# Optimization experiments

Hardware: AMD Instinct MI355X
Metric: run time of the kernel (lower is better)

## Reference

```python
import jax, jax.numpy as jnp
import numpy as np

N_USER = 50000
N_ITEM = 50000
D_IN = 128
D_OUT = 128
N_EDGE = 600000


def _sage(x_src, x_dst, ei, Wl, bl, Wr):
    # PyG SAGEConv: out = lin_l(mean_{j in N(i)} x_j) + lin_r(x_i)
    # lin_l has bias, lin_r has no bias. Weights are [out, in].
    src, dst = ei[0], ei[1]
    n_dst = x_dst.shape[0]
    msg = x_src[src]                                            # [E, D_in] gather
    agg = jax.ops.segment_sum(msg, dst, num_segments=n_dst)     # [N_dst, D_in]
    cnt = jax.ops.segment_sum(jnp.ones((ei.shape[1],), x_src.dtype), dst,
                              num_segments=n_dst)
    mean = agg / jnp.maximum(cnt, 1.0)[:, None]                 # isolated nodes -> 0
    return mean @ Wl.T + bl + x_dst @ Wr.T


def setup_inputs() -> dict:
    key = jax.random.key(0)
    ks = jax.random.split(key, 16)
    inp = {
        "x_user": jax.random.normal(ks[0], (N_USER, D_IN), jnp.float32),
        "x_item": jax.random.normal(ks[1], (N_ITEM, D_IN), jnp.float32),
        "ei_rates": jax.random.randint(ks[2], (2, N_EDGE), 0, N_USER, jnp.int64 if jax.config.jax_enable_x64 else jnp.int32),
        "ei_rev": jax.random.randint(ks[3], (2, N_EDGE), 0, N_USER, jnp.int64 if jax.config.jax_enable_x64 else jnp.int32),
        "ei_follows": jax.random.randint(ks[4], (2, N_EDGE), 0, N_USER, jnp.int64 if jax.config.jax_enable_x64 else jnp.int32),
    }
    s = 1.0 / np.sqrt(D_IN)
    names = ["rates", "rev", "fol"]
    for i, nm in enumerate(names):
        inp[f"Wl_{nm}"] = jax.random.uniform(ks[5 + 3 * i], (D_OUT, D_IN), jnp.float32, -s, s)
        inp[f"bl_{nm}"] = jax.random.uniform(ks[6 + 3 * i], (D_OUT,), jnp.float32, -s, s)
        inp[f"Wr_{nm}"] = jax.random.uniform(ks[7 + 3 * i], (D_OUT, D_IN), jnp.float32, -s, s)
    return inp


def reference(x_user, x_item, ei_rates, ei_rev, ei_follows,
              Wl_rates, bl_rates, Wr_rates,
              Wl_rev, bl_rev, Wr_rev,
              Wl_fol, bl_fol, Wr_fol):
    # relation (user -rates-> item): src=user, dst=item
    out_item = _sage(x_user, x_item, ei_rates, Wl_rates, bl_rates, Wr_rates)
    # relation (item -rev_rates-> user): src=item, dst=user
    out_user_rev = _sage(x_item, x_user, ei_rev, Wl_rev, bl_rev, Wr_rev)
    # relation (user -follows-> user)
    out_user_fol = _sage(x_user, x_user, ei_follows, Wl_fol, bl_fol, Wr_fol)
    # HeteroConv aggr='mean': average relation outputs per dst node type
    out_user = (out_user_rev + out_user_fol) * 0.5
    return out_user, out_item
```

## Files before the change

kernel.cpp:

```cpp
#include <hip/hip_runtime.h>

#define D 128
#define NBB 392

typedef __attribute__((ext_vector_type(8))) short bf16x8;
typedef __attribute__((ext_vector_type(4))) float f32x4;

__device__ inline unsigned short f2bf(float f) {
  unsigned u = __builtin_bit_cast(unsigned, f);
  unsigned r = u + 0x7FFFu + ((u >> 16) & 1u);
  return (unsigned short)(r >> 16);
}
__device__ inline float bf2f(unsigned short b) {
  unsigned u = ((unsigned)b) << 16;
  return __builtin_bit_cast(float, u);
}

__global__ void __launch_bounds__(256) conv2_kernel(
    const float* __restrict__ xu, const float* __restrict__ xi,
    unsigned short* __restrict__ xbu, unsigned short* __restrict__ xbi,
    int n4u, int n4i) {
  int i = blockIdx.x * 256 + threadIdx.x;
  const float* x;
  unsigned short* xb;
  if (i < n4u) { x = xu; xb = xbu; }
  else { i -= n4u; if (i >= n4i) return; x = xi; xb = xbi; }
  float4 v = ((const float4*)x)[i];
  ushort4 o;
  o.x = f2bf(v.x); o.y = f2bf(v.y); o.z = f2bf(v.z); o.w = f2bf(v.w);
  ((ushort4*)xb)[i] = o;
}

struct Rel3 { const int* ei[3]; int ne[3]; int nb[3]; };

__global__ void __launch_bounds__(256) bhist_kernel(Rel3 R, int* __restrict__ bh) {
  int b = blockIdx.x, rel = 0;
  while (b >= R.nb[rel]) { b -= R.nb[rel]; rel++; }
  __shared__ int lh[NBB];
  for (int t = threadIdx.x; t < NBB; t += 256) lh[t] = 0;
  __syncthreads();
  const int ne = R.ne[rel];
  const int* dsts = R.ei[rel] + ne;
  const int base = b * 2048;
#pragma unroll
  for (int k = 0; k < 8; k++) {
    int i = base + k * 256 + threadIdx.x;
    if (i < ne) atomicAdd(&lh[dsts[i] >> 7], 1);
  }
  __syncthreads();
  for (int t = threadIdx.x; t < NBB; t += 256)
    if (lh[t]) atomicAdd(&bh[rel * NBB + t], lh[t]);
}

__global__ void __launch_bounds__(192) scanb_kernel(const int* __restrict__ bh,
                                                    int* __restrict__ bbase,
                                                    int* __restrict__ bcur, int nbkt) {
  int w = threadIdx.x >> 6, l = threadIdx.x & 63;
  if (w >= 3) return;
  const int off = w * NBB;
  int v[7];
  int s0 = 0;
#pragma unroll
  for (int k = 0; k < 7; k++) {
    int idx = l * 7 + k;
    v[k] = (idx < nbkt) ? bh[off + idx] : 0;
    s0 += v[k];
  }
  int s = s0;
  for (int dlt = 1; dlt < 64; dlt <<= 1) {
    int t = __shfl_up(s, dlt);
    if (l >= dlt) s += t;
  }
  int run = s - s0;
#pragma unroll
  for (int k = 0; k < 7; k++) {
    int idx = l * 7 + k;
    if (idx < nbkt) { bbase[off + idx] = run; bcur[off + idx] = run; run += v[k]; }
  }
  if (l == 63) bbase[off + nbkt] = run;
}

struct PArgs { const int* ei[3]; int ne[3]; int nb[3]; unsigned* part[3]; };

__global__ void __launch_bounds__(256) part_kernel(PArgs P, int* __restrict__ bcur,
                                                   int nbkt) {
  int b = blockIdx.x, rel = 0;
  while (b >= P.nb[rel]) { b -= P.nb[rel]; rel++; }
  const int ne = P.ne[rel];
  const int* src = P.ei[rel];
  const int* dst = src + ne;
  const int base = b * 4096;
  const int tn = min(4096, ne - base);
  __shared__ int lh[NBB], lscan[NBB], gb[NBB], lcur[NBB];
  __shared__ uint2 pairs[4096];
  const int tid = threadIdx.x;
  for (int t = tid; t < NBB; t += 256) lh[t] = 0;
  __syncthreads();
#pragma unroll
  for (int k = 0; k < 16; k++) {
    int i = base + k * 256 + tid;
    if (i < ne) atomicAdd(&lh[dst[i] >> 7], 1);
  }
  __syncthreads();
  if (tid < 64) {
    int v[7];
    int s0 = 0;
#pragma unroll
    for (int k = 0; k < 7; k++) {
      int idx = tid * 7 + k;
      v[k] = (idx < NBB) ? lh[idx] : 0;
      s0 += v[k];
    }
    int s = s0;
    for (int dlt = 1; dlt < 64; dlt <<= 1) {
      int t = __shfl_up(s, dlt);
      if (tid >= dlt) s += t;
    }
    int run = s - s0;
#pragma unroll
    for (int k = 0; k < 7; k++) {
      int idx = tid * 7 + k;
      if (idx < NBB) { lscan[idx] = run; run += v[k]; }
    }
  }
  __syncthreads();
  for (int t = tid; t < nbkt; t += 256) {
    gb[t] = atomicAdd(&bcur[rel * NBB + t], lh[t]);
    lcur[t] = lscan[t];
  }
  __syncthreads();
#pragma unroll
  for (int k = 0; k < 16; k++) {
    int i = base + k * 256 + tid;
    if (i < ne) {
      int d = dst[i];
      int slot = atomicAdd(&lcur[d >> 7], 1);
      pairs[slot] = (uint2){(unsigned)src[i], (unsigned)d};
    }
  }
  __syncthreads();
  unsigned* __restrict__ out = P.part[rel];
#pragma unroll
  for (int k = 0; k < 16; k++) {
    int slot = k * 256 + tid;
    if (slot < tn) {
      uint2 p = pairs[slot];
      int bin = (int)(p.y >> 7);
      out[gb[bin] + (slot - lscan[bin])] = p.x | ((p.y & 127u) << 25);
    }
  }
}

struct BAArgs {
  const unsigned* part[3];
  const unsigned short* xb[3];
  unsigned short* mean[3];
  int m[3];
};

__global__ void __launch_bounds__(256) bagg_kernel(BAArgs A, const int* __restrict__ bbase,
                                                   int nbkt) {
  const int rel = blockIdx.x / nbkt;
  const int b = blockIdx.x - rel * nbkt;
  const int bs = bbase[rel * NBB + b];
  const int be = bbase[rel * NBB + b + 1];
  const int n = be - bs;
  const unsigned* __restrict__ pp = A.part[rel] + bs;
  const unsigned short* __restrict__ x = A.xb[rel];
  unsigned short* __restrict__ mean = A.mean[rel];
  const int m = A.m[rel];
  const int tid = threadIdx.x;
  const int w = tid >> 6, lane = tid & 63;
  const size_t loff = lane * 2;
  __shared__ unsigned sorted[4096];
  __shared__ int lcnt[128], lofs[128], lcur[128];

  if (n <= 4096) {
    if (tid < 128) lcnt[tid] = 0;
    __syncthreads();
    for (int i = tid; i < n; i += 256) atomicAdd(&lcnt[pp[i] >> 25], 1);
    __syncthreads();
    if (tid < 64) {
      int v0 = lcnt[2 * tid], v1 = lcnt[2 * tid + 1];
      int s0 = v0 + v1, s = s0;
      for (int dlt = 1; dlt < 64; dlt <<= 1) {
        int t = __shfl_up(s, dlt);
        if (tid >= dlt) s += t;
      }
      int ex = s - s0;
      lofs[2 * tid] = ex;
      lofs[2 * tid + 1] = ex + v0;
    }
    __syncthreads();
    if (tid < 128) lcur[tid] = lofs[tid];
    __syncthreads();
    for (int i = tid; i < n; i += 256) {
      unsigned p = pp[i];
      int slot = atomicAdd(&lcur[p >> 25], 1);
      sorted[slot] = p & 0x1FFFFFFu;
    }
    __syncthreads();
    for (int r = w; r < 128; r += 4) {
      int gdst = b * 128 + r;
      if (gdst >= m) break;
      const int beg = lofs[r], end = lcur[r];
      float a0 = 0.f, a1 = 0.f, b0 = 0.f, b1 = 0.f;
      float c0 = 0.f, c1 = 0.f, d0 = 0.f, d1 = 0.f;
      int j = beg;
      for (; j + 4 <= end; j += 4) {
        unsigned s0 = sorted[j], s1 = sorted[j + 1], s2 = sorted[j + 2], s3 = sorted[j + 3];
        unsigned v0 = *(const unsigned*)(x + (size_t)s0 * D + loff);
        unsigned v1 = *(const unsigned*)(x + (size_t)s1 * D + loff);
        unsigned v2 = *(const unsigned*)(x + (size_t)s2 * D + loff);
        unsigned v3 = *(const unsigned*)(x + (size_t)s3 * D + loff);
        a0 += bf2f((unsigned short)(v0 & 0xFFFFu)); a1 += bf2f((unsigned short)(v0 >> 16));
        b0 += bf2f((unsigned short)(v1 & 0xFFFFu)); b1 += bf2f((unsigned short)(v1 >> 16));
        c0 += bf2f((unsigned short)(v2 & 0xFFFFu)); c1 += bf2f((unsigned short)(v2 >> 16));
        d0 += bf2f((unsigned short)(v3 & 0xFFFFu)); d1 += bf2f((unsigned short)(v3 >> 16));
      }
      for (; j < end; j++) {
        unsigned s = sorted[j];
        unsigned v = *(const unsigned*)(x + (size_t)s * D + loff);
        a0 += bf2f((unsigned short)(v & 0xFFFFu)); a1 += bf2f((unsigned short)(v >> 16));
      }
      a0 += (b0 + c0) + d0;
      a1 += (b1 + c1) + d1;
      float inv = 1.0f / (float)max(end - beg, 1);
      unsigned o = (unsigned)f2bf(a0 * inv) | ((unsigned)f2bf(a1 * inv) << 16);
      *(unsigned*)(mean + (size_t)gdst * D + loff) = o;
    }
  } else {
    for (int r = w; r < 128; r += 4) {
      int gdst = b * 128 + r;
      if (gdst >= m) break;
      float a0 = 0.f, a1 = 0.f;
      int cnt = 0;
      for (int j = 0; j < n; j++) {
        unsigned p = pp[j];
        if ((int)(p >> 25) == r) {
          unsigned v = *(const unsigned*)(x + (size_t)(p & 0x1FFFFFFu) * D + loff);
          a0 += bf2f((unsigned short)(v & 0xFFFFu));
          a1 += bf2f((unsigned short)(v >> 16));
          cnt++;
        }
      }
      float inv = 1.0f / (float)max(cnt, 1);
      unsigned o = (unsigned)f2bf(a0 * inv) | ((unsigned)f2bf(a1 * inv) << 16);
      *(unsigned*)(mean + (size_t)gdst * D + loff) = o;
    }
  }
}

__global__ void __launch_bounds__(384) prep_kernel(
    const float* __restrict__ Wl_rates, const float* __restrict__ Wr_rates, const float* __restrict__ bl_rates,
    const float* __restrict__ Wl_rev, const float* __restrict__ Wr_rev, const float* __restrict__ bl_rev,
    const float* __restrict__ Wl_fol, const float* __restrict__ Wr_fol, const float* __restrict__ bl_fol,
    unsigned short* __restrict__ Wb_user, unsigned short* __restrict__ Wb_item,
    float* __restrict__ b_user, float* __restrict__ b_item) {
  int n = blockIdx.x;
  int k = threadIdx.x;
  float v;
  if (k < 128)      v = 0.5f * Wl_rev[n * 128 + k];
  else if (k < 256) v = 0.5f * Wl_fol[n * 128 + (k - 128)];
  else              v = 0.5f * (Wr_rev[n * 128 + (k - 256)] + Wr_fol[n * 128 + (k - 256)]);
  Wb_user[n * 384 + k] = f2bf(v);
  if (k < 256) {
    float w = (k < 128) ? Wl_rates[n * 128 + k] : Wr_rates[n * 128 + (k - 128)];
    Wb_item[n * 256 + k] = f2bf(w);
  }
  if (n == 0 && k < 128) {
    b_item[k] = bl_rates[k];
    b_user[k] = 0.5f * (bl_rev[k] + bl_fol[k]);
  }
}

struct BSrcs { const unsigned short* s[3]; };
struct GemmArgs {
  BSrcs su, si;
  const unsigned short* wbU; const unsigned short* wbI;
  const float* bU; const float* bI;
  float* outU; float* outI;
  int MU, MI, nbU;
};

__global__ void __launch_bounds__(256) gemm2_kernel(GemmArgs A) {
  const bool isU = (int)blockIdx.x < A.nbU;
  const int bid = isU ? blockIdx.x : blockIdx.x - A.nbU;
  const BSrcs S = isU ? A.su : A.si;
  const unsigned short* __restrict__ Wb = isU ? A.wbU : A.wbI;
  const int K = isU ? 384 : 256;
  const float* __restrict__ bias = isU ? A.bU : A.bI;
  float* __restrict__ out = isU ? A.outU : A.outI;
  const int M = isU ? A.MU : A.MI;

  __shared__ __align__(16) unsigned short As[128][72];
  __shared__ __align__(16) unsigned short Ws[128][72];
  const int tid = threadIdx.x;
  const int lane = tid & 63;
  const int wave = tid >> 6;
  const int wr = (wave >> 1) * 64;
  const int wc = (wave & 1) * 64;
  const int l15 = lane & 15;
  const int quad = lane >> 4;
  const int m0 = bid * 128;

  f32x4 acc[4][4];
#pragma unroll
  for (int r = 0; r < 4; r++)
#pragma unroll
    for (int c = 0; c < 4; c++) acc[r][c] = (f32x4){0.f, 0.f, 0.f, 0.f};

  const int srow = tid >> 1, shalf = tid & 1;
  const int nchunks = K >> 6;
  for (int ch = 0; ch < nchunks; ch++) {
    const unsigned short* sp = S.s[ch >> 1];
    const int coff = (ch & 1) << 6;
    {
      int mm = min(m0 + srow, M - 1);
      const uint4* g = (const uint4*)(sp + (size_t)mm * D + coff + shalf * 32);
      uint4* ld = (uint4*)(&As[srow][shalf * 32]);
      ld[0] = g[0]; ld[1] = g[1]; ld[2] = g[2]; ld[3] = g[3];
    }
    {
      const uint4* g = (const uint4*)(Wb + (size_t)srow * K + ch * 64 + shalf * 32);
      uint4* ld = (uint4*)(&Ws[srow][shalf * 32]);
      ld[0] = g[0]; ld[1] = g[1]; ld[2] = g[2]; ld[3] = g[3];
    }
    __syncthreads();
#pragma unroll
    for (int kk = 0; kk < 64; kk += 32) {
      const int kb = kk + quad * 8;
      bf16x8 a0 = *(const bf16x8*)&As[wr + l15][kb];
      bf16x8 a1 = *(const bf16x8*)&As[wr + 16 + l15][kb];
      bf16x8 a2 = *(const bf16x8*)&As[wr + 32 + l15][kb];
      bf16x8 a3 = *(const bf16x8*)&As[wr + 48 + l15][kb];
      bf16x8 b0 = *(const bf16x8*)&Ws[wc + l15][kb];
      bf16x8 b1 = *(const bf16x8*)&Ws[wc + 16 + l15][kb];
      bf16x8 b2 = *(const bf16x8*)&Ws[wc + 32 + l15][kb];
      bf16x8 b3 = *(const bf16x8*)&Ws[wc + 48 + l15][kb];
      acc[0][0] = __builtin_amdgcn_mfma_f32_16x16x32_bf16(a0, b0, acc[0][0], 0, 0, 0);
      acc[0][1] = __builtin_amdgcn_mfma_f32_16x16x32_bf16(a0, b1, acc[0][1], 0, 0, 0);
      acc[0][2] = __builtin_amdgcn_mfma_f32_16x16x32_bf16(a0, b2, acc[0][2], 0, 0, 0);
      acc[0][3] = __builtin_amdgcn_mfma_f32_16x16x32_bf16(a0, b3, acc[0][3], 0, 0, 0);
      acc[1][0] = __builtin_amdgcn_mfma_f32_16x16x32_bf16(a1, b0, acc[1][0], 0, 0, 0);
      acc[1][1] = __builtin_amdgcn_mfma_f32_16x16x32_bf16(a1, b1, acc[1][1], 0, 0, 0);
      acc[1][2] = __builtin_amdgcn_mfma_f32_16x16x32_bf16(a1, b2, acc[1][2], 0, 0, 0);
      acc[1][3] = __builtin_amdgcn_mfma_f32_16x16x32_bf16(a1, b3, acc[1][3], 0, 0, 0);
      acc[2][0] = __builtin_amdgcn_mfma_f32_16x16x32_bf16(a2, b0, acc[2][0], 0, 0, 0);
      acc[2][1] = __builtin_amdgcn_mfma_f32_16x16x32_bf16(a2, b1, acc[2][1], 0, 0, 0);
      acc[2][2] = __builtin_amdgcn_mfma_f32_16x16x32_bf16(a2, b2, acc[2][2], 0, 0, 0);
      acc[2][3] = __builtin_amdgcn_mfma_f32_16x16x32_bf16(a2, b3, acc[2][3], 0, 0, 0);
      acc[3][0] = __builtin_amdgcn_mfma_f32_16x16x32_bf16(a3, b0, acc[3][0], 0, 0, 0);
      acc[3][1] = __builtin_amdgcn_mfma_f32_16x16x32_bf16(a3, b1, acc[3][1], 0, 0, 0);
      acc[3][2] = __builtin_amdgcn_mfma_f32_16x16x32_bf16(a3, b2, acc[3][2], 0, 0, 0);
      acc[3][3] = __builtin_amdgcn_mfma_f32_16x16x32_bf16(a3, b3, acc[3][3], 0, 0, 0);
    }
    __syncthreads();
  }
#pragma unroll
  for (int c = 0; c < 4; c++) {
    const int n = wc + c * 16 + l15;
    const float bv = bias[n];
#pragma unroll
    for (int r = 0; r < 4; r++) {
      const int mrow = m0 + wr + r * 16 + quad * 4;
#pragma unroll
      for (int i = 0; i < 4; i++) {
        if (mrow + i < M) out[(size_t)(mrow + i) * D + n] = acc[r][c][i] + bv;
      }
    }
  }
}

extern "C" void kernel_launch(void* const* d_in, const int* in_sizes, int n_in,
                              void* d_out, int out_size, void* d_ws, size_t ws_size,
                              hipStream_t stream) {
  const float* x_user   = (const float*)d_in[0];
  const float* x_item   = (const float*)d_in[1];
  const int*   ei_rates = (const int*)d_in[2];
  const int*   ei_rev   = (const int*)d_in[3];
  const int*   ei_fol   = (const int*)d_in[4];
  const float* Wl_rates = (const float*)d_in[5];
  const float* bl_rates = (const float*)d_in[6];
  const float* Wr_rates = (const float*)d_in[7];
  const float* Wl_rev   = (const float*)d_in[8];
  const float* bl_rev   = (const float*)d_in[9];
  const float* Wr_rev   = (const float*)d_in[10];
  const float* Wl_fol   = (const float*)d_in[11];
  const float* bl_fol   = (const float*)d_in[12];
  const float* Wr_fol   = (const float*)d_in[13];

  const int NU = in_sizes[0] / D;
  const int NI = in_sizes[1] / D;
  const int E_rates = in_sizes[2] / 2;
  const int E_rev   = in_sizes[3] / 2;
  const int E_fol   = in_sizes[4] / 2;
  const int nbkt = ((NU > NI ? NU : NI) + 127) / 128;

  char* wsb = (char*)d_ws;
  size_t off = 0;
  auto take = [&](size_t bytes) {
    char* p = wsb + off;
    off += (bytes + 15) & ~(size_t)15;
    return p;
  };
  int* bhist = (int*)take(3 * NBB * 4);
  const size_t zero_bytes = off;
  int* bbase = (int*)take(3 * NBB * 4);
  int* bcur  = (int*)take(3 * NBB * 4);
  unsigned* part_rates = (unsigned*)take((size_t)E_rates * 4);
  unsigned* part_rev   = (unsigned*)take((size_t)E_rev * 4);
  unsigned* part_fol   = (unsigned*)take((size_t)E_fol * 4);
  unsigned short* xb_user    = (unsigned short*)take((size_t)NU * D * 2);
  unsigned short* xb_item    = (unsigned short*)take((size_t)NI * D * 2);
  unsigned short* mean_rates = (unsigned short*)take((size_t)NI * D * 2);
  unsigned short* mean_rev   = (unsigned short*)take((size_t)NU * D * 2);
  unsigned short* mean_fol   = (unsigned short*)take((size_t)NU * D * 2);
  unsigned short* Wb_user    = (unsigned short*)take(128 * 384 * 2);
  unsigned short* Wb_item    = (unsigned short*)take(128 * 256 * 2);
  float* b_user = (float*)take(128 * 4);
  float* b_item = (float*)take(128 * 4);

  hipMemsetAsync(d_ws, 0, zero_bytes, stream);
  prep_kernel<<<128, 384, 0, stream>>>(Wl_rates, Wr_rates, bl_rates,
                                       Wl_rev, Wr_rev, bl_rev,
                                       Wl_fol, Wr_fol, bl_fol,
                                       Wb_user, Wb_item, b_user, b_item);
  {
    int n4u = NU * D / 4, n4i = NI * D / 4;
    conv2_kernel<<<(n4u + n4i + 255) / 256, 256, 0, stream>>>(
        x_user, x_item, xb_user, xb_item, n4u, n4i);
  }

  Rel3 R;
  R.ei[0] = ei_rates; R.ne[0] = E_rates; R.nb[0] = (E_rates + 2047) / 2048;
  R.ei[1] = ei_rev;   R.ne[1] = E_rev;   R.nb[1] = (E_rev + 2047) / 2048;
  R.ei[2] = ei_fol;   R.ne[2] = E_fol;   R.nb[2] = (E_fol + 2047) / 2048;
  bhist_kernel<<<R.nb[0] + R.nb[1] + R.nb[2], 256, 0, stream>>>(R, bhist);

  scanb_kernel<<<1, 192, 0, stream>>>(bhist, bbase, bcur, nbkt);

  PArgs P;
  P.ei[0] = ei_rates; P.ne[0] = E_rates; P.nb[0] = (E_rates + 4095) / 4096; P.part[0] = part_rates;
  P.ei[1] = ei_rev;   P.ne[1] = E_rev;   P.nb[1] = (E_rev + 4095) / 4096;   P.part[1] = part_rev;
  P.ei[2] = ei_fol;   P.ne[2] = E_fol;   P.nb[2] = (E_fol + 4095) / 4096;   P.part[2] = part_fol;
  part_kernel<<<P.nb[0] + P.nb[1] + P.nb[2], 256, 0, stream>>>(P, bcur, nbkt);

  BAArgs BA;
  BA.part[0] = part_rates; BA.xb[0] = xb_user; BA.mean[0] = mean_rates; BA.m[0] = NI;
  BA.part[1] = part_rev;   BA.xb[1] = xb_item; BA.mean[1] = mean_rev;   BA.m[1] = NU;
  BA.part[2] = part_fol;   BA.xb[2] = xb_user; BA.mean[2] = mean_fol;   BA.m[2] = NU;
  bagg_kernel<<<3 * nbkt, 256, 0, stream>>>(BA, bbase, nbkt);

  GemmArgs gma;
  gma.su.s[0] = mean_rev;   gma.su.s[1] = mean_fol; gma.su.s[2] = xb_user;
  gma.si.s[0] = mean_rates; gma.si.s[1] = xb_item;  gma.si.s[2] = nullptr;
  gma.wbU = Wb_user; gma.wbI = Wb_item;
  gma.bU = b_user;   gma.bI = b_item;
  gma.outU = (float*)d_out;
  gma.outI = (float*)d_out + (size_t)NU * D;
  gma.MU = NU; gma.MI = NI;
  gma.nbU = (NU + 127) / 128;
  const int nbI = (NI + 127) / 128;
  gemm2_kernel<<<gma.nbU + nbI, 256, 0, stream>>>(gma);
}
```

Before: 314.0 us.

## Merge setup kernels into one launch and interleave two rows in bucket aggregation

```diff
diff --git a/kernel.cpp b/kernel.cpp
--- a/kernel.cpp
+++ b/kernel.cpp
@@ -16,40 +16,71 @@
   return __builtin_bit_cast(float, u);
 }
 
-__global__ void __launch_bounds__(256) conv2_kernel(
-    const float* __restrict__ xu, const float* __restrict__ xi,
-    unsigned short* __restrict__ xbu, unsigned short* __restrict__ xbi,
-    int n4u, int n4i) {
-  int i = blockIdx.x * 256 + threadIdx.x;
-  const float* x;
-  unsigned short* xb;
-  if (i < n4u) { x = xu; xb = xbu; }
-  else { i -= n4u; if (i >= n4i) return; x = xi; xb = xbi; }
-  float4 v = ((const float4*)x)[i];
-  ushort4 o;
-  o.x = f2bf(v.x); o.y = f2bf(v.y); o.z = f2bf(v.z); o.w = f2bf(v.w);
-  ((ushort4*)xb)[i] = o;
-}
-
-struct Rel3 { const int* ei[3]; int ne[3]; int nb[3]; };
-
-__global__ void __launch_bounds__(256) bhist_kernel(Rel3 R, int* __restrict__ bh) {
-  int b = blockIdx.x, rel = 0;
-  while (b >= R.nb[rel]) { b -= R.nb[rel]; rel++; }
-  __shared__ int lh[NBB];
-  for (int t = threadIdx.x; t < NBB; t += 256) lh[t] = 0;
-  __syncthreads();
-  const int ne = R.ne[rel];
-  const int* dsts = R.ei[rel] + ne;
-  const int base = b * 2048;
-#pragma unroll
-  for (int k = 0; k < 8; k++) {
-    int i = base + k * 256 + threadIdx.x;
-    if (i < ne) atomicAdd(&lh[dsts[i] >> 7], 1);
-  }
-  __syncthreads();
-  for (int t = threadIdx.x; t < NBB; t += 256)
-    if (lh[t]) atomicAdd(&bh[rel * NBB + t], lh[t]);
+struct SetupArgs {
+  const float* xu; const float* xi;
+  unsigned short* xbu; unsigned short* xbi;
+  int n4u, n4i, nbConv;
+  const int* ei[3]; int ne[3]; int nbh[3]; int nbHist;
+  int* bh;
+  const float* Wl_rates; const float* Wr_rates; const float* bl_rates;
+  const float* Wl_rev;   const float* Wr_rev;   const float* bl_rev;
+  const float* Wl_fol;   const float* Wr_fol;   const float* bl_fol;
+  unsigned short* Wb_user; unsigned short* Wb_item;
+  float* b_user; float* b_item;
+};
+
+__global__ void __launch_bounds__(256) setup_kernel(SetupArgs S) {
+  const int tid = threadIdx.x;
+  int b = blockIdx.x;
+  if (b < S.nbConv) {
+    int i = b * 256 + tid;
+    const float* x;
+    unsigned short* xb;
+    if (i < S.n4u) { x = S.xu; xb = S.xbu; }
+    else { i -= S.n4u; if (i >= S.n4i) return; x = S.xi; xb = S.xbi; }
+    float4 v = ((const float4*)x)[i];
+    ushort4 o;
+    o.x = f2bf(v.x); o.y = f2bf(v.y); o.z = f2bf(v.z); o.w = f2bf(v.w);
+    ((ushort4*)xb)[i] = o;
+    return;
+  }
+  b -= S.nbConv;
+  if (b < S.nbHist) {
+    int rel = 0;
+    while (b >= S.nbh[rel]) { b -= S.nbh[rel]; rel++; }
+    __shared__ int lh[NBB];
+    for (int t = tid; t < NBB; t += 256) lh[t] = 0;
+    __syncthreads();
+    const int ne = S.ne[rel];
+    const int* dsts = S.ei[rel] + ne;
+    const int base = b * 2048;
+#pragma unroll
+    for (int k = 0; k < 8; k++) {
+      int i = base + k * 256 + tid;
+      if (i < ne) atomicAdd(&lh[dsts[i] >> 7], 1);
+    }
+    __syncthreads();
+    for (int t = tid; t < NBB; t += 256)
+      if (lh[t]) atomicAdd(&S.bh[rel * NBB + t], lh[t]);
+    return;
+  }
+  b -= S.nbHist;
+  int idx = b * 256 + tid;
+  if (idx >= 128 * 384) return;
+  int n = idx / 384, k = idx - n * 384;
+  float v;
+  if (k < 128)      v = 0.5f * S.Wl_rev[n * 128 + k];
+  else if (k < 256) v = 0.5f * S.Wl_fol[n * 128 + (k - 128)];
+  else              v = 0.5f * (S.Wr_rev[n * 128 + (k - 256)] + S.Wr_fol[n * 128 + (k - 256)]);
+  S.Wb_user[n * 384 + k] = f2bf(v);
+  if (k < 256) {
+    float w = (k < 128) ? S.Wl_rates[n * 128 + k] : S.Wr_rates[n * 128 + (k - 128)];
+    S.Wb_item[n * 256 + k] = f2bf(w);
+  }
+  if (idx < 128) {
+    S.b_item[idx] = S.bl_rates[idx];
+    S.b_user[idx] = 0.5f * (S.bl_rev[idx] + S.bl_fol[idx]);
+  }
 }
 
 __global__ void __launch_bounds__(192) scanb_kernel(const int* __restrict__ bh,
@@ -175,61 +206,7 @@
   __shared__ unsigned sorted[4096];
   __shared__ int lcnt[128], lofs[128], lcur[128];
 
-  if (n <= 4096) {
-    if (tid < 128) lcnt[tid] = 0;
-    __syncthreads();
-    for (int i = tid; i < n; i += 256) atomicAdd(&lcnt[pp[i] >> 25], 1);
-    __syncthreads();
-    if (tid < 64) {
-      int v0 = lcnt[2 * tid], v1 = lcnt[2 * tid + 1];
-      int s0 = v0 + v1, s = s0;
-      for (int dlt = 1; dlt < 64; dlt <<= 1) {
-        int t = __shfl_up(s, dlt);
-        if (tid >= dlt) s += t;
-      }
-      int ex = s - s0;
-      lofs[2 * tid] = ex;
-      lofs[2 * tid + 1] = ex + v0;
-    }
-    __syncthreads();
-    if (tid < 128) lcur[tid] = lofs[tid];
-    __syncthreads();
-    for (int i = tid; i < n; i += 256) {
-      unsigned p = pp[i];
-      int slot = atomicAdd(&lcur[p >> 25], 1);
-      sorted[slot] = p & 0x1FFFFFFu;
-    }
-    __syncthreads();
-    for (int r = w; r < 128; r += 4) {
-      int gdst = b * 128 + r;
-      if (gdst >= m) break;
-      const int beg = lofs[r], end = lcur[r];
-      float a0 = 0.f, a1 = 0.f, b0 = 0.f, b1 = 0.f;
-      float c0 = 0.f, c1 = 0.f, d0 = 0.f, d1 = 0.f;
-      int j = beg;
-      for (; j + 4 <= end; j += 4) {
-        unsigned s0 = sorted[j], s1 = sorted[j + 1], s2 = sorted[j + 2], s3 = sorted[j + 3];
-        unsigned v0 = *(const unsigned*)(x + (size_t)s0 * D + loff);
-        unsigned v1 = *(const unsigned*)(x + (size_t)s1 * D + loff);
-        unsigned v2 = *(const unsigned*)(x + (size_t)s2 * D + loff);
-        unsigned v3 = *(const unsigned*)(x + (size_t)s3 * D + loff);
-        a0 += bf2f((unsigned short)(v0 & 0xFFFFu)); a1 += bf2f((unsigned short)(v0 >> 16));
-        b0 += bf2f((unsigned short)(v1 & 0xFFFFu)); b1 += bf2f((unsigned short)(v1 >> 16));
-        c0 += bf2f((unsigned short)(v2 & 0xFFFFu)); c1 += bf2f((unsigned short)(v2 >> 16));
-        d0 += bf2f((unsigned short)(v3 & 0xFFFFu)); d1 += bf2f((unsigned short)(v3 >> 16));
-      }
-      for (; j < end; j++) {
-        unsigned s = sorted[j];
-        unsigned v = *(const unsigned*)(x + (size_t)s * D + loff);
-        a0 += bf2f((unsigned short)(v & 0xFFFFu)); a1 += bf2f((unsigned short)(v >> 16));
-      }
-      a0 += (b0 + c0) + d0;
-      a1 += (b1 + c1) + d1;
-      float inv = 1.0f / (float)max(end - beg, 1);
-      unsigned o = (unsigned)f2bf(a0 * inv) | ((unsigned)f2bf(a1 * inv) << 16);
-      *(unsigned*)(mean + (size_t)gdst * D + loff) = o;
-    }
-  } else {
+  if (n > 4096) {
     for (int r = w; r < 128; r += 4) {
       int gdst = b * 128 + r;
       if (gdst >= m) break;
@@ -248,29 +225,112 @@
       unsigned o = (unsigned)f2bf(a0 * inv) | ((unsigned)f2bf(a1 * inv) << 16);
       *(unsigned*)(mean + (size_t)gdst * D + loff) = o;
     }
-  }
-}
-
-__global__ void __launch_bounds__(384) prep_kernel(
-    const float* __restrict__ Wl_rates, const float* __restrict__ Wr_rates, const float* __restrict__ bl_rates,
-    const float* __restrict__ Wl_rev, const float* __restrict__ Wr_rev, const float* __restrict__ bl_rev,
-    const float* __restrict__ Wl_fol, const float* __restrict__ Wr_fol, const float* __restrict__ bl_fol,
-    unsigned short* __restrict__ Wb_user, unsigned short* __restrict__ Wb_item,
-    float* __restrict__ b_user, float* __restrict__ b_item) {
-  int n = blockIdx.x;
-  int k = threadIdx.x;
-  float v;
-  if (k < 128)      v = 0.5f * Wl_rev[n * 128 + k];
-  else if (k < 256) v = 0.5f * Wl_fol[n * 128 + (k - 128)];
-  else              v = 0.5f * (Wr_rev[n * 128 + (k - 256)] + Wr_fol[n * 128 + (k - 256)]);
-  Wb_user[n * 384 + k] = f2bf(v);
-  if (k < 256) {
-    float w = (k < 128) ? Wl_rates[n * 128 + k] : Wr_rates[n * 128 + (k - 128)];
-    Wb_item[n * 256 + k] = f2bf(w);
-  }
-  if (n == 0 && k < 128) {
-    b_item[k] = bl_rates[k];
-    b_user[k] = 0.5f * (bl_rev[k] + bl_fol[k]);
+    return;
+  }
+
+  if (tid < 128) lcnt[tid] = 0;
+  __syncthreads();
+  for (int i = tid; i < n; i += 256) atomicAdd(&lcnt[pp[i] >> 25], 1);
+  __syncthreads();
+  if (tid < 64) {
+    int v0 = lcnt[2 * tid], v1 = lcnt[2 * tid + 1];
+    int s0 = v0 + v1, s = s0;
+    for (int dlt = 1; dlt < 64; dlt <<= 1) {
+      int t = __shfl_up(s, dlt);
+      if (tid >= dlt) s += t;
+    }
+    int ex = s - s0;
+    lofs[2 * tid] = ex;
+    lofs[2 * tid + 1] = ex + v0;
+  }
+  __syncthreads();
+  if (tid < 128) lcur[tid] = lofs[tid];
+  __syncthreads();
+  for (int i = tid; i < n; i += 256) {
+    unsigned p = pp[i];
+    int slot = atomicAdd(&lcur[p >> 25], 1);
+    sorted[slot] = p & 0x1FFFFFFu;
+  }
+  __syncthreads();
+
+  for (int r = w; r < 128; r += 8) {
+    const int rA = r, rB = r + 4;
+    const int gA = b * 128 + rA, gB = b * 128 + rB;
+    if (gA >= m) break;
+    const bool doB = gB < m;
+    int jA = lofs[rA];
+    const int eA = lcur[rA];
+    int jB = doB ? lofs[rB] : 0;
+    const int eB = doB ? lcur[rB] : 0;
+    float aA0=0,aA1=0,bA0=0,bA1=0,cA0=0,cA1=0,dA0=0,dA1=0;
+    float aB0=0,aB1=0,bB0=0,bB1=0,cB0=0,cB1=0,dB0=0,dB1=0;
+    while (jA + 4 <= eA && jB + 4 <= eB) {
+      unsigned sA0 = sorted[jA], sA1 = sorted[jA+1], sA2 = sorted[jA+2], sA3 = sorted[jA+3];
+      unsigned sB0 = sorted[jB], sB1 = sorted[jB+1], sB2 = sorted[jB+2], sB3 = sorted[jB+3];
+      unsigned vA0 = *(const unsigned*)(x + (size_t)sA0 * D + loff);
+      unsigned vA1 = *(const unsigned*)(x + (size_t)sA1 * D + loff);
+      unsigned vA2 = *(const unsigned*)(x + (size_t)sA2 * D + loff);
+      unsigned vA3 = *(const unsigned*)(x + (size_t)sA3 * D + loff);
+      unsigned vB0 = *(const unsigned*)(x + (size_t)sB0 * D + loff);
+      unsigned vB1 = *(const unsigned*)(x + (size_t)sB1 * D + loff);
+      unsigned vB2 = *(const unsigned*)(x + (size_t)sB2 * D + loff);
+      unsigned vB3 = *(const unsigned*)(x + (size_t)sB3 * D + loff);
+      aA0 += bf2f((unsigned short)(vA0 & 0xFFFFu)); aA1 += bf2f((unsigned short)(vA0 >> 16));
+      bA0 += bf2f((unsigned short)(vA1 & 0xFFFFu)); bA1 += bf2f((unsigned short)(vA1 >> 16));
+      cA0 += bf2f((unsigned short)(vA2 & 0xFFFFu)); cA1 += bf2f((unsigned short)(vA2 >> 16));
+      dA0 += bf2f((unsigned short)(vA3 & 0xFFFFu)); dA1 += bf2f((unsigned short)(vA3 >> 16));
+      aB0 += bf2f((unsigned short)(vB0 & 0xFFFFu)); aB1 += bf2f((unsigned short)(vB0 >> 16));
+      bB0 += bf2f((unsigned short)(vB1 & 0xFFFFu)); bB1 += bf2f((unsigned short)(vB1 >> 16));
+      cB0 += bf2f((unsigned short)(vB2 & 0xFFFFu)); cB1 += bf2f((unsigned short)(vB2 >> 16));
+      dB0 += bf2f((unsigned short)(vB3 & 0xFFFFu)); dB1 += bf2f((unsigned short)(vB3 >> 16));
+      jA += 4; jB += 4;
+    }
+    for (; jA + 4 <= eA; jA += 4) {
+      unsigned s0 = sorted[jA], s1 = sorted[jA+1], s2 = sorted[jA+2], s3 = sorted[jA+3];
+      unsigned v0 = *(const unsigned*)(x + (size_t)s0 * D + loff);
+      unsigned v1 = *(const unsigned*)(x + (size_t)s1 * D + loff);
+      unsigned v2 = *(const unsigned*)(x + (size_t)s2 * D + loff);
+      unsigned v3 = *(const unsigned*)(x + (size_t)s3 * D + loff);
+      aA0 += bf2f((unsigned short)(v0 & 0xFFFFu)); aA1 += bf2f((unsigned short)(v0 >> 16));
+      bA0 += bf2f((unsigned short)(v1 & 0xFFFFu)); bA1 += bf2f((unsigned short)(v1 >> 16));
+      cA0 += bf2f((unsigned short)(v2 & 0xFFFFu)); cA1 += bf2f((unsigned short)(v2 >> 16));
+      dA0 += bf2f((unsigned short)(v3 & 0xFFFFu)); dA1 += bf2f((unsigned short)(v3 >> 16));
+    }
+    for (; jA < eA; jA++) {
+      unsigned s = sorted[jA];
+      unsigned v = *(const unsigned*)(x + (size_t)s * D + loff);
+      aA0 += bf2f((unsigned short)(v & 0xFFFFu)); aA1 += bf2f((unsigned short)(v >> 16));
+    }
+    for (; jB + 4 <= eB; jB += 4) {
+      unsigned s0 = sorted[jB], s1 = sorted[jB+1], s2 = sorted[jB+2], s3 = sorted[jB+3];
+      unsigned v0 = *(const unsigned*)(x + (size_t)s0 * D + loff);
+      unsigned v1 = *(const unsigned*)(x + (size_t)s1 * D + loff);
+      unsigned v2 = *(const unsigned*)(x + (size_t)s2 * D + loff);
+      unsigned v3 = *(const unsigned*)(x + (size_t)s3 * D + loff);
+      aB0 += bf2f((unsigned short)(v0 & 0xFFFFu)); aB1 += bf2f((unsigned short)(v0 >> 16));
+      bB0 += bf2f((unsigned short)(v1 & 0xFFFFu)); bB1 += bf2f((unsigned short)(v1 >> 16));
+      cB0 += bf2f((unsigned short)(v2 & 0xFFFFu)); cB1 += bf2f((unsigned short)(v2 >> 16));
+      dB0 += bf2f((unsigned short)(v3 & 0xFFFFu)); dB1 += bf2f((unsigned short)(v3 >> 16));
+    }
+    for (; jB < eB; jB++) {
+      unsigned s = sorted[jB];
+      unsigned v = *(const unsigned*)(x + (size_t)s * D + loff);
+      aB0 += bf2f((unsigned short)(v & 0xFFFFu)); aB1 += bf2f((unsigned short)(v >> 16));
+    }
+    {
+      float v0 = (aA0 + bA0) + (cA0 + dA0);
+      float v1 = (aA1 + bA1) + (cA1 + dA1);
+      float inv = 1.0f / (float)max(eA - lofs[rA], 1);
+      unsigned o = (unsigned)f2bf(v0 * inv) | ((unsigned)f2bf(v1 * inv) << 16);
+      *(unsigned*)(mean + (size_t)gA * D + loff) = o;
+    }
+    if (doB) {
+      float v0 = (aB0 + bB0) + (cB0 + dB0);
+      float v1 = (aB1 + bB1) + (cB1 + dB1);
+      float inv = 1.0f / (float)max(eB - lofs[rB], 1);
+      unsigned o = (unsigned)f2bf(v0 * inv) | ((unsigned)f2bf(v1 * inv) << 16);
+      *(unsigned*)(mean + (size_t)gB * D + loff) = o;
+    }
   }
 }
 
@@ -422,21 +482,23 @@
   float* b_item = (float*)take(128 * 4);
 
   hipMemsetAsync(d_ws, 0, zero_bytes, stream);
-  prep_kernel<<<128, 384, 0, stream>>>(Wl_rates, Wr_rates, bl_rates,
-                                       Wl_rev, Wr_rev, bl_rev,
-                                       Wl_fol, Wr_fol, bl_fol,
-                                       Wb_user, Wb_item, b_user, b_item);
-  {
-    int n4u = NU * D / 4, n4i = NI * D / 4;
-    conv2_kernel<<<(n4u + n4i + 255) / 256, 256, 0, stream>>>(
-        x_user, x_item, xb_user, xb_item, n4u, n4i);
-  }
-
-  Rel3 R;
-  R.ei[0] = ei_rates; R.ne[0] = E_rates; R.nb[0] = (E_rates + 2047) / 2048;
-  R.ei[1] = ei_rev;   R.ne[1] = E_rev;   R.nb[1] = (E_rev + 2047) / 2048;
-  R.ei[2] = ei_fol;   R.ne[2] = E_fol;   R.nb[2] = (E_fol + 2047) / 2048;
-  bhist_kernel<<<R.nb[0] + R.nb[1] + R.nb[2], 256, 0, stream>>>(R, bhist);
+
+  SetupArgs SA;
+  SA.xu = x_user; SA.xi = x_item; SA.xbu = xb_user; SA.xbi = xb_item;
+  SA.n4u = NU * D / 4; SA.n4i = NI * D / 4;
+  SA.nbConv = (SA.n4u + SA.n4i + 255) / 256;
+  SA.ei[0] = ei_rates; SA.ne[0] = E_rates; SA.nbh[0] = (E_rates + 2047) / 2048;
+  SA.ei[1] = ei_rev;   SA.ne[1] = E_rev;   SA.nbh[1] = (E_rev + 2047) / 2048;
+  SA.ei[2] = ei_fol;   SA.ne[2] = E_fol;   SA.nbh[2] = (E_fol + 2047) / 2048;
+  SA.nbHist = SA.nbh[0] + SA.nbh[1] + SA.nbh[2];
+  SA.bh = bhist;
+  SA.Wl_rates = Wl_rates; SA.Wr_rates = Wr_rates; SA.bl_rates = bl_rates;
+  SA.Wl_rev = Wl_rev; SA.Wr_rev = Wr_rev; SA.bl_rev = bl_rev;
+  SA.Wl_fol = Wl_fol; SA.Wr_fol = Wr_fol; SA.bl_fol = bl_fol;
+  SA.Wb_user = Wb_user; SA.Wb_item = Wb_item;
+  SA.b_user = b_user; SA.b_item = b_item;
+  const int nbPrep = (128 * 384 + 255) / 256;
+  setup_kernel<<<SA.nbConv + SA.nbHist + nbPrep, 256, 0, stream>>>(SA);
 
   scanb_kernel<<<1, 192, 0, stream>>>(bhist, bbase, bcur, nbkt);
 
```

Result: faster. 306.1 us (-2.5%).
